# Kernel tuning notes

Measured on AMD Instinct MI355X. Metric: run time of the kernel, lower is better.

## Reference

```python
import jax, jax.numpy as jnp
import numpy as np

B, N, K, F_IN, F_OUT = 8, 2048, 32, 256, 256


def setup_inputs() -> dict:
    key = jax.random.key(0)
    ks = jax.random.split(key, 8)
    x = jax.random.normal(ks[0], (B, N, F_IN), dtype=jnp.float32)
    idx_neib = jax.random.randint(ks[1], (N, K), 0, N, dtype=jnp.int32)
    # Linear params (torch nn.Linear stores weight as [out, in])
    lim_x = np.sqrt(2.0) * np.sqrt(6.0 / (F_IN + F_OUT))  # xavier_uniform, gain=relu
    Wx_w = jax.random.uniform(ks[2], (F_OUT, F_IN), jnp.float32, -lim_x, lim_x)
    Wx_b = jnp.zeros((F_OUT,), jnp.float32)
    Wn_w = jax.random.uniform(ks[3], (F_OUT, F_IN), jnp.float32, -lim_x, lim_x)
    Wn_b = jnp.zeros((F_OUT,), jnp.float32)
    gamma = jnp.ones((2 * F_OUT,), jnp.float32)
    beta = jnp.zeros((2 * F_OUT,), jnp.float32)
    return {"x": x, "idx_neib": idx_neib, "Wx_w": Wx_w, "Wx_b": Wx_b,
            "Wn_w": Wn_w, "Wn_b": Wn_b, "gamma": gamma, "beta": beta}


def reference(x, idx_neib, Wx_w, Wx_b, Wn_w, Wn_b, gamma, beta):
    # Gather neighbor features: [B, N, K, F] then mean over the K neighbors.
    x_neib = jnp.take(x, idx_neib, axis=1).mean(axis=2)  # [B, N, F]
    # Dual linear projections (weights stored [out, in] as in torch).
    h_self = jnp.einsum('bnf,of->bno', x, Wx_w) + Wx_b
    h_nei = jnp.einsum('bnf,of->bno', x_neib, Wn_w) + Wn_b
    h = jnp.concatenate([h_self, h_nei], axis=2)          # [B, N, 2*out]
    # F.normalize(p=2, dim=2): divide by max(||h||_2, 1e-12)
    nrm = jnp.sqrt(jnp.sum(h * h, axis=2, keepdims=True))
    h = h / jnp.maximum(nrm, 1e-12)
    h = jax.nn.relu(h)
    # BatchNorm1d over channel dim (training mode: batch stats over B and N,
    # biased variance), eps=1e-5.
    mu = h.mean(axis=(0, 1))
    var = jnp.mean((h - mu) ** 2, axis=(0, 1))
    h = (h - mu) * jax.lax.rsqrt(var + 1e-5) * gamma + beta
    return h
```

## Files before the change

kernel.cpp:

```cpp
#include <hip/hip_runtime.h>
#include <stdint.h>

#define BB 8
#define NN 2048
#define KK 32
#define FIN 256
#define FOUT 256
#define CC 512
#define MM (BB*NN)
#define RB 32
#define NBLK (MM/RB)
#define LDA 264

typedef __attribute__((ext_vector_type(8))) short short8;
typedef __attribute__((ext_vector_type(4))) float f32x4;

__device__ __forceinline__ unsigned short f2bf(float f) {
    union { float f; unsigned u; } v; v.f = f;
    unsigned u = v.u;
    return (unsigned short)((u + 0x7FFFu + ((u >> 16) & 1u)) >> 16);
}
__device__ __forceinline__ float bf2f(unsigned short s) {
    union { unsigned u; float f; } v; v.u = ((unsigned)s) << 16;
    return v.f;
}

__global__ void k_prep(const float* __restrict__ Wx, const float* __restrict__ Wxb,
                       const float* __restrict__ Wn, const float* __restrict__ Wnb,
                       unsigned short* __restrict__ Wc, float* __restrict__ bc) {
    int gid = blockIdx.x * 256 + threadIdx.x;
    int o = gid >> 8, k = gid & 255;
    float w = (o < FOUT) ? Wx[o * FIN + k] : Wn[(o - FOUT) * FIN + k];
    Wc[gid] = f2bf(w);
    if (gid < CC) bc[gid] = (gid < FOUT) ? Wxb[gid] : Wnb[gid - FOUT];
}

__global__ void k_conv(const float* __restrict__ x, unsigned short* __restrict__ xb) {
    int gid = blockIdx.x * 256 + threadIdx.x;
    float4 v = ((const float4*)x)[gid];
    ushort4 o; o.x = f2bf(v.x); o.y = f2bf(v.y); o.z = f2bf(v.z); o.w = f2bf(v.w);
    ((ushort4*)xb)[gid] = o;
}

__global__ void k_gather(const unsigned short* __restrict__ xb,
                         const int* __restrict__ idx,
                         unsigned short* __restrict__ xnb) {
    int wave = threadIdx.x >> 6;
    int lane = threadIdx.x & 63;
    int r = blockIdx.x * 4 + wave;
    int b = r >> 11, n = r & 2047;
    const int* ip = idx + n * KK;
    const unsigned short* xbb = xb + (size_t)b * NN * FIN + lane * 4;
    float a0 = 0.f, a1 = 0.f, a2 = 0.f, a3 = 0.f;
    #pragma unroll 8
    for (int k = 0; k < KK; ++k) {
        int j = ip[k];
        ushort4 v = *(const ushort4*)(xbb + (size_t)j * FIN);
        a0 += bf2f(v.x); a1 += bf2f(v.y); a2 += bf2f(v.z); a3 += bf2f(v.w);
    }
    const float s = 1.0f / (float)KK;
    ushort4 o; o.x = f2bf(a0 * s); o.y = f2bf(a1 * s); o.z = f2bf(a2 * s); o.w = f2bf(a3 * s);
    *(ushort4*)(xnb + (size_t)r * FIN + lane * 4) = o;
}

__global__ __launch_bounds__(256, 2)
void k_gemm(const unsigned short* __restrict__ xb,
            const unsigned short* __restrict__ xnb,
            const unsigned short* __restrict__ Wc,
            const float* __restrict__ bc,
            unsigned short* __restrict__ h,
            float* __restrict__ psum, float* __restrict__ psq) {
    __shared__ unsigned short As[2][RB * LDA];
    __shared__ float sqpart[4][RB];
    __shared__ float rnorm[RB];

    const int tid  = threadIdx.x;
    const int w    = tid >> 6;
    const int lane = tid & 63;
    const int quad = lane >> 4;
    const int l16  = lane & 15;
    const int r0   = blockIdx.x * RB;

    {
        const uint4* gs = (const uint4*)(xb  + (size_t)r0 * FIN);
        const uint4* gn = (const uint4*)(xnb + (size_t)r0 * FIN);
        #pragma unroll
        for (int i = 0; i < 4; ++i) {
            int e = tid + i * 256;
            int row = e >> 5, col8 = e & 31;
            *(uint4*)&As[0][row * LDA + col8 * 8] = gs[e];
            *(uint4*)&As[1][row * LDA + col8 * 8] = gn[e];
        }
    }
    __syncthreads();

    const unsigned short* A = As[w >> 1];
    const int cb = w * 128;

    f32x4 acc[2][8];
    #pragma unroll
    for (int mt = 0; mt < 2; ++mt)
        #pragma unroll
        for (int nt = 0; nt < 8; ++nt) acc[mt][nt] = (f32x4){0.f, 0.f, 0.f, 0.f};

    const unsigned short* Bp = Wc + (size_t)(cb + l16) * FIN + quad * 8;
    const unsigned short* Ap = A + (size_t)l16 * LDA + quad * 8;

    #pragma unroll
    for (int k0 = 0; k0 < FIN; k0 += 32) {
        short8 a0 = *(const short8*)(Ap + k0);
        short8 a1 = *(const short8*)(Ap + 16 * LDA + k0);
        short8 bfr[8];
        #pragma unroll
        for (int nt = 0; nt < 8; ++nt)
            bfr[nt] = *(const short8*)(Bp + (size_t)nt * 16 * FIN + k0);
        #pragma unroll
        for (int nt = 0; nt < 8; ++nt) {
            acc[0][nt] = __builtin_amdgcn_mfma_f32_16x16x32_bf16(a0, bfr[nt], acc[0][nt], 0, 0, 0);
            acc[1][nt] = __builtin_amdgcn_mfma_f32_16x16x32_bf16(a1, bfr[nt], acc[1][nt], 0, 0, 0);
        }
    }

    float bcv[8];
    #pragma unroll
    for (int nt = 0; nt < 8; ++nt) bcv[nt] = bc[cb + nt * 16 + l16];

    float rsq[2][4] = {{0.f,0.f,0.f,0.f},{0.f,0.f,0.f,0.f}};
    #pragma unroll
    for (int mt = 0; mt < 2; ++mt)
        #pragma unroll
        for (int nt = 0; nt < 8; ++nt)
            #pragma unroll
            for (int r = 0; r < 4; ++r) {
                float v = acc[mt][nt][r] + bcv[nt];
                acc[mt][nt][r] = v;
                rsq[mt][r] += v * v;
            }
    #pragma unroll
    for (int off = 1; off < 16; off <<= 1)
        #pragma unroll
        for (int mt = 0; mt < 2; ++mt)
            #pragma unroll
            for (int r = 0; r < 4; ++r)
                rsq[mt][r] += __shfl_xor(rsq[mt][r], off, 64);
    if (l16 == 0) {
        #pragma unroll
        for (int mt = 0; mt < 2; ++mt)
            #pragma unroll
            for (int r = 0; r < 4; ++r)
                sqpart[w][mt * 16 + quad * 4 + r] = rsq[mt][r];
    }
    __syncthreads();
    if (tid < RB) {
        float tot = sqpart[0][tid] + sqpart[1][tid] + sqpart[2][tid] + sqpart[3][tid];
        rnorm[tid] = 1.0f / fmaxf(sqrtf(tot), 1e-12f);
    }
    __syncthreads();

    float csum[8] = {0.f,0.f,0.f,0.f,0.f,0.f,0.f,0.f};
    float csq [8] = {0.f,0.f,0.f,0.f,0.f,0.f,0.f,0.f};
    #pragma unroll
    for (int mt = 0; mt < 2; ++mt) {
        #pragma unroll
        for (int r = 0; r < 4; ++r) {
            int row = mt * 16 + quad * 4 + r;
            float rn = rnorm[row];
            unsigned short* hp = h + (size_t)(r0 + row) * CC + cb + l16;
            #pragma unroll
            for (int nt = 0; nt < 8; ++nt) {
                float v = fmaxf(acc[mt][nt][r] * rn, 0.0f);
                hp[nt * 16] = f2bf(v);
                csum[nt] += v;
                csq [nt] += v * v;
            }
        }
    }
    #pragma unroll
    for (int off = 16; off < 64; off <<= 1)
        #pragma unroll
        for (int nt = 0; nt < 8; ++nt) {
            csum[nt] += __shfl_xor(csum[nt], off, 64);
            csq [nt] += __shfl_xor(csq [nt], off, 64);
        }
    if (quad == 0) {
        #pragma unroll
        for (int nt = 0; nt < 8; ++nt) {
            int c = cb + nt * 16 + l16;
            psum[(size_t)c * NBLK + blockIdx.x] = csum[nt];
            psq [(size_t)c * NBLK + blockIdx.x] = csq [nt];
        }
    }
}

__global__ void k_stats(const float* __restrict__ psum, const float* __restrict__ psq,
                        const float* __restrict__ gamma, const float* __restrict__ beta,
                        float* __restrict__ ss) {
    __shared__ float ps[4], pq[4];
    int c = blockIdx.x, t = threadIdx.x;
    float s = psum[(size_t)c * NBLK + t] + psum[(size_t)c * NBLK + 256 + t];
    float q = psq [(size_t)c * NBLK + t] + psq [(size_t)c * NBLK + 256 + t];
    #pragma unroll
    for (int off = 32; off; off >>= 1) { s += __shfl_xor(s, off, 64); q += __shfl_xor(q, off, 64); }
    int w = t >> 6, lane = t & 63;
    if (lane == 0) { ps[w] = s; pq[w] = q; }
    __syncthreads();
    if (t == 0) {
        float S = ps[0] + ps[1] + ps[2] + ps[3];
        float Q = pq[0] + pq[1] + pq[2] + pq[3];
        const float inv = 1.0f / (float)MM;
        float mu  = S * inv;
        float var = fmaxf(Q * inv - mu * mu, 0.0f);
        float sc  = gamma[c] * rsqrtf(var + 1e-5f);
        ss[c]      = sc;
        ss[CC + c] = beta[c] - mu * sc;
    }
}

__global__ void k_apply(const unsigned short* __restrict__ h,
                        const float* __restrict__ ss,
                        float* __restrict__ out) {
    int gid = blockIdx.x * 256 + threadIdx.x;
    int c0 = (gid * 4) & (CC - 1);
    ushort4 hv = ((const ushort4*)h)[gid];
    float4 sc = *(const float4*)(ss + c0);
    float4 sh = *(const float4*)(ss + CC + c0);
    float4 o;
    o.x = bf2f(hv.x) * sc.x + sh.x;
    o.y = bf2f(hv.y) * sc.y + sh.y;
    o.z = bf2f(hv.z) * sc.z + sh.z;
    o.w = bf2f(hv.w) * sc.w + sh.w;
    ((float4*)out)[gid] = o;
}

extern "C" void kernel_launch(void* const* d_in, const int* in_sizes, int n_in,
                              void* d_out, int out_size, void* d_ws, size_t ws_size,
                              hipStream_t stream) {
    const float* x     = (const float*)d_in[0];
    const int*   idx   = (const int*)  d_in[1];
    const float* Wx_w  = (const float*)d_in[2];
    const float* Wx_b  = (const float*)d_in[3];
    const float* Wn_w  = (const float*)d_in[4];
    const float* Wn_b  = (const float*)d_in[5];
    const float* gamma = (const float*)d_in[6];
    const float* beta  = (const float*)d_in[7];
    float* out = (float*)d_out;

    char* p = (char*)d_ws;
    unsigned short* xb  = (unsigned short*)p; p += (size_t)MM * FIN * 2;
    unsigned short* xnb = (unsigned short*)p; p += (size_t)MM * FIN * 2;
    unsigned short* Wc  = (unsigned short*)p; p += (size_t)CC * FIN * 2;
    float* bc           = (float*)p;          p += (size_t)CC * 4;
    unsigned short* h   = (unsigned short*)p; p += (size_t)MM * CC * 2;
    float* psum         = (float*)p;          p += (size_t)CC * NBLK * 4;
    float* psq          = (float*)p;          p += (size_t)CC * NBLK * 4;
    float* ss           = (float*)p;          p += (size_t)2 * CC * 4;

    hipLaunchKernelGGL(k_prep,   dim3(512),  dim3(256), 0, stream, Wx_w, Wx_b, Wn_w, Wn_b, Wc, bc);
    hipLaunchKernelGGL(k_conv,   dim3(4096), dim3(256), 0, stream, x, xb);
    hipLaunchKernelGGL(k_gather, dim3(4096), dim3(256), 0, stream, xb, idx, xnb);
    hipLaunchKernelGGL(k_gemm,   dim3(NBLK), dim3(256), 0, stream, xb, xnb, Wc, bc, h, psum, psq);
    hipLaunchKernelGGL(k_stats,  dim3(CC),   dim3(256), 0, stream, psum, psq, gamma, beta, ss);
    hipLaunchKernelGGL(k_apply,  dim3(8192), dim3(256), 0, stream, h, ss, out);
}
```

Measured before the change: 146.2 us.

## Fuse prep, convert and gather into one kernel gathering fp32 directly

Merges the weight-prep, x-to-bf16 conversion and neighbour-gather kernels into one launch, split by block-index range. The gather now reads fp32 x directly instead of waiting for the bf16 copy, which removes the dependency and two launches. Gather blocks are reordered so the 8 batches sharing one neighbour list sit in adjacent blocks, which should improve index reuse. In exchange the gather reads twice the bytes per neighbour, and the GEMM k-loop unroll drops from full to 2.

```diff
diff --git a/kernel.cpp b/kernel.cpp
--- a/kernel.cpp
+++ b/kernel.cpp
@@ -25,42 +25,43 @@
     return v.f;
 }
 
-__global__ void k_prep(const float* __restrict__ Wx, const float* __restrict__ Wxb,
-                       const float* __restrict__ Wn, const float* __restrict__ Wnb,
-                       unsigned short* __restrict__ Wc, float* __restrict__ bc) {
-    int gid = blockIdx.x * 256 + threadIdx.x;
-    int o = gid >> 8, k = gid & 255;
-    float w = (o < FOUT) ? Wx[o * FIN + k] : Wn[(o - FOUT) * FIN + k];
-    Wc[gid] = f2bf(w);
-    if (gid < CC) bc[gid] = (gid < FOUT) ? Wxb[gid] : Wnb[gid - FOUT];
-}
-
-__global__ void k_conv(const float* __restrict__ x, unsigned short* __restrict__ xb) {
-    int gid = blockIdx.x * 256 + threadIdx.x;
-    float4 v = ((const float4*)x)[gid];
-    ushort4 o; o.x = f2bf(v.x); o.y = f2bf(v.y); o.z = f2bf(v.z); o.w = f2bf(v.w);
-    ((ushort4*)xb)[gid] = o;
-}
-
-__global__ void k_gather(const unsigned short* __restrict__ xb,
-                         const int* __restrict__ idx,
-                         unsigned short* __restrict__ xnb) {
-    int wave = threadIdx.x >> 6;
-    int lane = threadIdx.x & 63;
-    int r = blockIdx.x * 4 + wave;
-    int b = r >> 11, n = r & 2047;
-    const int* ip = idx + n * KK;
-    const unsigned short* xbb = xb + (size_t)b * NN * FIN + lane * 4;
-    float a0 = 0.f, a1 = 0.f, a2 = 0.f, a3 = 0.f;
-    #pragma unroll 8
-    for (int k = 0; k < KK; ++k) {
-        int j = ip[k];
-        ushort4 v = *(const ushort4*)(xbb + (size_t)j * FIN);
-        a0 += bf2f(v.x); a1 += bf2f(v.y); a2 += bf2f(v.z); a3 += bf2f(v.w);
-    }
-    const float s = 1.0f / (float)KK;
-    ushort4 o; o.x = f2bf(a0 * s); o.y = f2bf(a1 * s); o.z = f2bf(a2 * s); o.w = f2bf(a3 * s);
-    *(ushort4*)(xnb + (size_t)r * FIN + lane * 4) = o;
+__global__ void k_pre(const float* __restrict__ x, const int* __restrict__ idx,
+                      const float* __restrict__ Wx, const float* __restrict__ Wxb,
+                      const float* __restrict__ Wn, const float* __restrict__ Wnb,
+                      unsigned short* __restrict__ xb, unsigned short* __restrict__ xnb,
+                      unsigned short* __restrict__ Wc, float* __restrict__ bc) {
+    const int blk = blockIdx.x;
+    const int tid = threadIdx.x;
+    if (blk < 4096) {
+        int b = blk & 7;
+        int n = (blk >> 3) * 4 + (tid >> 6);
+        int lane = tid & 63;
+        const int* ip = idx + n * KK;
+        const float* xbb = x + (size_t)b * NN * FIN + lane * 4;
+        float a0 = 0.f, a1 = 0.f, a2 = 0.f, a3 = 0.f;
+        #pragma unroll 8
+        for (int k = 0; k < KK; ++k) {
+            int j = ip[k];
+            float4 v = *(const float4*)(xbb + (size_t)j * FIN);
+            a0 += v.x; a1 += v.y; a2 += v.z; a3 += v.w;
+        }
+        const float s = 1.0f / (float)KK;
+        ushort4 o; o.x = f2bf(a0 * s); o.y = f2bf(a1 * s); o.z = f2bf(a2 * s); o.w = f2bf(a3 * s);
+        *(ushort4*)(xnb + ((size_t)b * NN + n) * FIN + lane * 4) = o;
+    } else if (blk < 8192) {
+        int c = blk - 4096;
+        int b = c & 7, chunk = c >> 3;
+        size_t f4 = (size_t)b * (NN * FIN / 4) + chunk * 256 + tid;
+        float4 v = ((const float4*)x)[f4];
+        ushort4 o; o.x = f2bf(v.x); o.y = f2bf(v.y); o.z = f2bf(v.z); o.w = f2bf(v.w);
+        ((ushort4*)xb)[f4] = o;
+    } else {
+        int gid = (blk - 8192) * 256 + tid;
+        int o = gid >> 8, k = gid & 255;
+        float w = (o < FOUT) ? Wx[o * FIN + k] : Wn[(o - FOUT) * FIN + k];
+        Wc[gid] = f2bf(w);
+        if (gid < CC) bc[gid] = (gid < FOUT) ? Wxb[gid] : Wnb[gid - FOUT];
+    }
 }
 
 __global__ __launch_bounds__(256, 2)
@@ -106,7 +107,7 @@
     const unsigned short* Bp = Wc + (size_t)(cb + l16) * FIN + quad * 8;
     const unsigned short* Ap = A + (size_t)l16 * LDA + quad * 8;
 
-    #pragma unroll
+    #pragma unroll 2
     for (int k0 = 0; k0 < FIN; k0 += 32) {
         short8 a0 = *(const short8*)(Ap + k0);
         short8 a1 = *(const short8*)(Ap + 16 * LDA + k0);
@@ -255,10 +256,9 @@
     float* psq          = (float*)p;          p += (size_t)CC * NBLK * 4;
     float* ss           = (float*)p;          p += (size_t)2 * CC * 4;
 
-    hipLaunchKernelGGL(k_prep,   dim3(512),  dim3(256), 0, stream, Wx_w, Wx_b, Wn_w, Wn_b, Wc, bc);
-    hipLaunchKernelGGL(k_conv,   dim3(4096), dim3(256), 0, stream, x, xb);
-    hipLaunchKernelGGL(k_gather, dim3(4096), dim3(256), 0, stream, xb, idx, xnb);
-    hipLaunchKernelGGL(k_gemm,   dim3(NBLK), dim3(256), 0, stream, xb, xnb, Wc, bc, h, psum, psq);
-    hipLaunchKernelGGL(k_stats,  dim3(CC),   dim3(256), 0, stream, psum, psq, gamma, beta, ss);
-    hipLaunchKernelGGL(k_apply,  dim3(8192), dim3(256), 0, stream, h, ss, out);
-}
+    hipLaunchKernelGGL(k_pre,   dim3(8704), dim3(256), 0, stream,
+                       x, idx, Wx_w, Wx_b, Wn_w, Wn_b, xb, xnb, Wc, bc);
+    hipLaunchKernelGGL(k_gemm,  dim3(NBLK), dim3(256), 0, stream, xb, xnb, Wc, bc, h, psum, psq);
+    hipLaunchKernelGGL(k_stats, dim3(CC),   dim3(256), 0, stream, psum, psq, gamma, beta, ss);
+    hipLaunchKernelGGL(k_apply, dim3(8192), dim3(256), 0, stream, h, ss, out);
+}
```

After: 141.9 us. -3.0%, faster.
